# Performance work log

Measured on AMD Instinct MI355X. Metric: run time of the kernel, lower is better.

Reference implementation:

```python
import jax, jax.numpy as jnp
import numpy as np

IN_F, OUT_F, RANK = 4096, 4096, 1024
B, S_LEN = 4, 2048


def _dequant(data, scale, zp):
    # (int_data - zero_point) * scale, per-tensor scalar quantization
    return (data.astype(jnp.float32) - zp.astype(jnp.float32)) * scale.astype(jnp.float32)


def setup_inputs() -> dict:
    key = jax.random.key(0)
    ks = jax.random.split(key, 8)
    x = jax.random.normal(ks[0], (B, S_LEN, IN_F), dtype=jnp.float32)
    U_data = jax.random.randint(ks[1], (OUT_F, RANK), 0, 255, dtype=jnp.int32)
    S_data = jax.random.randint(ks[2], (RANK,), 0, 255, dtype=jnp.int32)
    Vh_data = jax.random.randint(ks[3], (RANK, IN_F), 0, 255, dtype=jnp.int32)
    bias = jax.random.normal(ks[4], (OUT_F,), dtype=jnp.float32)
    return {
        "x": x,
        "U_data": U_data,
        "U_scale": jnp.array([0.02], dtype=jnp.float32),
        "U_zp": jnp.array([128.0], dtype=jnp.float32),
        "S_data": S_data,
        "S_scale": jnp.array([0.05], dtype=jnp.float32),
        "S_zp": jnp.array([128.0], dtype=jnp.float32),
        "Vh_data": Vh_data,
        "Vh_scale": jnp.array([0.02], dtype=jnp.float32),
        "Vh_zp": jnp.array([128.0], dtype=jnp.float32),
        "bias": bias,
    }


def reference(x, U_data, U_scale, U_zp, S_data, S_scale, S_zp,
              Vh_data, Vh_scale, Vh_zp, bias):
    U = _dequant(U_data, U_scale, U_zp)     # [out, r]
    S = _dequant(S_data, S_scale, S_zp)     # [r]
    Vh = _dequant(Vh_data, Vh_scale, Vh_zp)  # [r, in]
    orig_shape = x.shape
    x_flat = x.reshape(-1, orig_shape[-1])  # [N, in]
    h = x_flat @ Vh.T                        # [N, r]
    h = h * S[None, :]
    y = h @ U.T                              # [N, out]
    y = y + bias
    return y.reshape(orig_shape[:-1] + (U.shape[0],))
```

## Files before the change

kernel.cpp:

```cpp
#include <hip/hip_runtime.h>
#include <stdint.h>

#define NROWS 8192
#define INF   4096
#define OUTF  4096
#define RNK   1024

typedef unsigned short u16;
typedef __attribute__((ext_vector_type(8))) short bf16x8;
typedef __attribute__((ext_vector_type(4))) float f32x4;
typedef __attribute__((ext_vector_type(8))) unsigned short u16x8;

__device__ __forceinline__ u16 f32_bf16(float f) {
  union { float f; uint32_t u; } v; v.f = f;
  return (u16)((v.u + 0x7FFF + ((v.u >> 16) & 1)) >> 16);
}


__global__ __launch_bounds__(256) void convert_x(const float* __restrict__ x,
                                                 u16* __restrict__ o) {
  int t = blockIdx.x * 256 + threadIdx.x;
  int e = t * 8;
  float4 a = *(const float4*)(x + e);
  float4 b = *(const float4*)(x + e + 4);
  u16x8 r;
  r[0] = f32_bf16(a.x); r[1] = f32_bf16(a.y); r[2] = f32_bf16(a.z); r[3] = f32_bf16(a.w);
  r[4] = f32_bf16(b.x); r[5] = f32_bf16(b.y); r[6] = f32_bf16(b.z); r[7] = f32_bf16(b.w);
  *(u16x8*)(o + e) = r;
}

__global__ __launch_bounds__(256) void dequant_vh(const int* __restrict__ vh,
                                                  const float* __restrict__ vs,
                                                  const float* __restrict__ vz,
                                                  const int* __restrict__ sd,
                                                  const float* __restrict__ ss,
                                                  const float* __restrict__ sz,
                                                  u16* __restrict__ o) {
  int t = blockIdx.x * 256 + threadIdx.x;
  int e = t * 4;
  int row = e >> 12;
  float sval = ((float)sd[row] - sz[0]) * ss[0];
  float sc = vs[0] * sval;
  float zp = vz[0];
  int4 d = *(const int4*)(vh + e);
  ushort4 r;
  r.x = f32_bf16(((float)d.x - zp) * sc);
  r.y = f32_bf16(((float)d.y - zp) * sc);
  r.z = f32_bf16(((float)d.z - zp) * sc);
  r.w = f32_bf16(((float)d.w - zp) * sc);
  *(ushort4*)(o + e) = r;
}

__global__ __launch_bounds__(256) void dequant_u(const int* __restrict__ ud,
                                                 const float* __restrict__ us,
                                                 const float* __restrict__ uz,
                                                 u16* __restrict__ o) {
  int t = blockIdx.x * 256 + threadIdx.x;
  int e = t * 4;
  float sc = us[0];
  float zp = uz[0];
  int4 d = *(const int4*)(ud + e);
  ushort4 r;
  r.x = f32_bf16(((float)d.x - zp) * sc);
  r.y = f32_bf16(((float)d.y - zp) * sc);
  r.z = f32_bf16(((float)d.z - zp) * sc);
  r.w = f32_bf16(((float)d.w - zp) * sc);
  *(ushort4*)(o + e) = r;
}


__device__ __forceinline__ void gl_lds16(const u16* g, u16* l) {
  __builtin_amdgcn_global_load_lds(
      (const __attribute__((address_space(1))) void*)g,
      (__attribute__((address_space(3))) void*)l, 16, 0, 0);
}

template <bool OUT_BF16, bool ADD_BIAS>
__global__ __launch_bounds__(256) void gemm_bt(const u16* __restrict__ A,
                                               const u16* __restrict__ B,
                                               void* __restrict__ Cv,
                                               const float* __restrict__ bias,
                                               const int N, const int K) {
  constexpr int BM = 128, BN = 128, BK = 64;
  __shared__ __attribute__((aligned(16))) u16 ldsA[BM * BK];
  __shared__ __attribute__((aligned(16))) u16 ldsB[BN * BK];

  const int tid  = threadIdx.x;
  const int lane = tid & 63;
  const int wave = tid >> 6;
  const int bm = blockIdx.y * BM;
  const int bn = blockIdx.x * BN;
  const int wm = (wave >> 1) * 64;
  const int wn = (wave & 1) * 64;

  f32x4 acc[4][4] = {};

  const int srow = tid >> 3;
  const int scol = (((tid & 7) ^ (srow & 7)) * 8);
  const int lcol = (tid & 7) * 8;
  const u16* gA = A + (bm + srow) * K + scol;
  const u16* gB = B + (bn + srow) * K + scol;
  u16* lA = ldsA + srow * BK + lcol;
  u16* lB = ldsB + srow * BK + lcol;

  for (int kt = 0; kt < K; kt += BK) {
#pragma unroll
    for (int i = 0; i < 4; ++i) {
      gl_lds16(gA + i * 32 * K + kt, lA + i * 32 * BK);
      gl_lds16(gB + i * 32 * K + kt, lB + i * 32 * BK);
    }
    __syncthreads();

    const int r  = lane & 15;
    const int kq = (lane >> 4) * 8;
#pragma unroll
    for (int ks = 0; ks < BK; ks += 32) {
      const int pcol = (((ks + kq) >> 3) ^ (r & 7)) << 3;
      bf16x8 af[4], bfr[4];
#pragma unroll
      for (int i = 0; i < 4; ++i)
        af[i] = *(const bf16x8*)(ldsA + (wm + i * 16 + r) * BK + pcol);
#pragma unroll
      for (int j = 0; j < 4; ++j)
        bfr[j] = *(const bf16x8*)(ldsB + (wn + j * 16 + r) * BK + pcol);
#pragma unroll
      for (int i = 0; i < 4; ++i)
#pragma unroll
        for (int j = 0; j < 4; ++j)
          acc[i][j] = __builtin_amdgcn_mfma_f32_16x16x32_bf16(af[i], bfr[j], acc[i][j], 0, 0, 0);
    }
    __syncthreads();
  }

  const int col0 = lane & 15;
  const int row0 = (lane >> 4) * 4;
#pragma unroll
  for (int i = 0; i < 4; ++i) {
#pragma unroll
    for (int j = 0; j < 4; ++j) {
      const int gcol = bn + wn + j * 16 + col0;
      float bv = 0.f;
      if (ADD_BIAS) bv = bias[gcol];
#pragma unroll
      for (int rr = 0; rr < 4; ++rr) {
        const int grow = bm + wm + i * 16 + row0 + rr;
        float v = acc[i][j][rr] + bv;
        if (OUT_BF16)
          ((u16*)Cv)[grow * N + gcol] = f32_bf16(v);
        else
          ((float*)Cv)[grow * N + gcol] = v;
      }
    }
  }
}


extern "C" void kernel_launch(void* const* d_in, const int* in_sizes, int n_in,
                              void* d_out, int out_size, void* d_ws, size_t ws_size,
                              hipStream_t stream) {
  const float* x        = (const float*)d_in[0];
  const int*   U_data   = (const int*)d_in[1];
  const float* U_scale  = (const float*)d_in[2];
  const float* U_zp     = (const float*)d_in[3];
  const int*   S_data   = (const int*)d_in[4];
  const float* S_scale  = (const float*)d_in[5];
  const float* S_zp     = (const float*)d_in[6];
  const int*   Vh_data  = (const int*)d_in[7];
  const float* Vh_scale = (const float*)d_in[8];
  const float* Vh_zp    = (const float*)d_in[9];
  const float* bias     = (const float*)d_in[10];
  float* out = (float*)d_out;

  char* ws = (char*)d_ws;
  u16* xb  = (u16*)ws;
  u16* vhb = (u16*)(ws + (size_t)67108864);
  u16* ub  = (u16*)(ws + (size_t)67108864 + 8388608);
  u16* hb  = (u16*)(ws + (size_t)67108864 + 16777216);

  convert_x<<<NROWS * INF / (8 * 256), 256, 0, stream>>>(x, xb);
  dequant_vh<<<RNK * INF / (4 * 256), 256, 0, stream>>>(Vh_data, Vh_scale, Vh_zp,
                                                        S_data, S_scale, S_zp, vhb);
  dequant_u<<<OUTF * RNK / (4 * 256), 256, 0, stream>>>(U_data, U_scale, U_zp, ub);

  gemm_bt<true, false><<<dim3(RNK / 128, NROWS / 128), 256, 0, stream>>>(
      xb, vhb, (void*)hb, nullptr, RNK, INF);
  gemm_bt<false, true><<<dim3(OUTF / 128, NROWS / 128), 256, 0, stream>>>(
      hb, ub, (void*)out, bias, OUTF, RNK);
}
```

Before: 425.6 us.

## Replace GEMM with 8-wave double-buffered pipelined kernel using larger tiles

Replaces the simple single-buffered 128x128 GEMM with a 512-thread, 256xBN tile kernel that double-buffers LDS and splits each K step into four phases. Each phase issues the async global-to-LDS loads for the next stage while running MFMAs on the current one, with explicit vmcnt waits, barriers and setprio. The aim is to hide global load latency and raise arithmetic intensity through larger tiles. In exchange it uses more LDS and registers and depends on correct hand-written wait counts.

```diff
diff --git a/kernel.cpp b/kernel.cpp
--- a/kernel.cpp
+++ b/kernel.cpp
@@ -75,83 +75,151 @@
       (__attribute__((address_space(3))) void*)l, 16, 0, 0);
 }
 
-template <bool OUT_BF16, bool ADD_BIAS>
-__global__ __launch_bounds__(256) void gemm_bt(const u16* __restrict__ A,
-                                               const u16* __restrict__ B,
-                                               void* __restrict__ Cv,
-                                               const float* __restrict__ bias,
-                                               const int N, const int K) {
-  constexpr int BM = 128, BN = 128, BK = 64;
-  __shared__ __attribute__((aligned(16))) u16 ldsA[BM * BK];
-  __shared__ __attribute__((aligned(16))) u16 ldsB[BN * BK];
+template <int VM> __device__ __forceinline__ void vm_wait() {
+  static_assert(VM == 3 || VM == 4, "unexpected vmcnt");
+  if constexpr (VM == 3) asm volatile("s_waitcnt vmcnt(3)" ::: "memory");
+  if constexpr (VM == 4) asm volatile("s_waitcnt vmcnt(4)" ::: "memory");
+}
+
+template <int BN, int K, int N, bool OUT_BF16, bool ADD_BIAS>
+__global__ __launch_bounds__(512, 2) void gemm8p(const u16* __restrict__ A,
+                                                 const u16* __restrict__ B,
+                                                 void* __restrict__ Cv,
+                                                 const float* __restrict__ bias) {
+  constexpr int BM = 256, BK = 64;
+  constexpr int WN = BN / 4;
+  constexpr int QJ = WN / 32;
+  constexpr int LB = (BN == 256) ? 2 : 1;
+  constexpr int NT = K / BK;
+  constexpr int AH = 128 * BK;
+  constexpr int BH = (BN / 2) * BK;
+
+  __shared__ __attribute__((aligned(16))) u16 ldsA[2 * 2 * AH];
+  __shared__ __attribute__((aligned(16))) u16 ldsB[2 * 2 * BH];
 
   const int tid  = threadIdx.x;
   const int lane = tid & 63;
   const int wave = tid >> 6;
-  const int bm = blockIdx.y * BM;
-  const int bn = blockIdx.x * BN;
-  const int wm = (wave >> 1) * 64;
-  const int wn = (wave & 1) * 64;
-
-  f32x4 acc[4][4] = {};
+  const int wm   = wave >> 2;
+  const int wn   = wave & 3;
+  const int bm   = blockIdx.y * BM;
+  const int bn   = blockIdx.x * BN;
 
   const int srow = tid >> 3;
-  const int scol = (((tid & 7) ^ (srow & 7)) * 8);
-  const int lcol = (tid & 7) * 8;
-  const u16* gA = A + (bm + srow) * K + scol;
-  const u16* gB = B + (bn + srow) * K + scol;
-  u16* lA = ldsA + srow * BK + lcol;
-  u16* lB = ldsB + srow * BK + lcol;
-
-  for (int kt = 0; kt < K; kt += BK) {
-#pragma unroll
-    for (int i = 0; i < 4; ++i) {
-      gl_lds16(gA + i * 32 * K + kt, lA + i * 32 * BK);
-      gl_lds16(gB + i * 32 * K + kt, lB + i * 32 * BK);
-    }
-    __syncthreads();
-
-    const int r  = lane & 15;
-    const int kq = (lane >> 4) * 8;
-#pragma unroll
-    for (int ks = 0; ks < BK; ks += 32) {
-      const int pcol = (((ks + kq) >> 3) ^ (r & 7)) << 3;
-      bf16x8 af[4], bfr[4];
-#pragma unroll
-      for (int i = 0; i < 4; ++i)
-        af[i] = *(const bf16x8*)(ldsA + (wm + i * 16 + r) * BK + pcol);
-#pragma unroll
-      for (int j = 0; j < 4; ++j)
-        bfr[j] = *(const bf16x8*)(ldsB + (wn + j * 16 + r) * BK + pcol);
-#pragma unroll
-      for (int i = 0; i < 4; ++i)
-#pragma unroll
-        for (int j = 0; j < 4; ++j)
-          acc[i][j] = __builtin_amdgcn_mfma_f32_16x16x32_bf16(af[i], bfr[j], acc[i][j], 0, 0, 0);
-    }
-    __syncthreads();
+  const int spc  = tid & 7;
+  const int sgc  = spc ^ (srow & 7);
+
+  const u16* gA = A + (size_t)(bm + srow) * K + sgc * 8;
+  const u16* gB = B + (size_t)(bn + srow) * K + sgc * 8;
+  u16* lA = ldsA + srow * BK + spc * 8;
+  u16* lB = ldsB + srow * BK + spc * 8;
+
+#define STAGE_A(buf, h, kt)                                                    \
+  { const u16* g_ = gA + (size_t)(h) * 128 * K + (kt);                         \
+    u16* l_ = lA + ((buf) * 2 + (h)) * AH;                                     \
+    gl_lds16(g_, l_);                                                          \
+    gl_lds16(g_ + (size_t)64 * K, l_ + 64 * BK); }
+
+#define STAGE_B(buf, h, kt)                                                    \
+  { const u16* g_ = gB + (size_t)(h) * (BN / 2) * K + (kt);                    \
+    u16* l_ = lB + ((buf) * 2 + (h)) * BH;                                     \
+    gl_lds16(g_, l_);                                                          \
+    if constexpr (LB == 2) gl_lds16(g_ + (size_t)64 * K, l_ + 64 * BK); }
+
+  const int r   = lane & 15;
+  const int kq  = (lane >> 4) * 8;
+  const int pc0 = (((kq) >> 3) ^ (r & 7)) << 3;
+  const int pc1 = (((32 + kq) >> 3) ^ (r & 7)) << 3;
+
+  f32x4 acc[2][2][4][QJ] = {};
+
+#define PHASE(buf, qm, qn, STAGE, VMW)                                         \
+  {                                                                            \
+    bf16x8 af[4][2], bfr[QJ][2];                                               \
+    const u16* abase = ldsA + ((buf) * 2 + (qm)) * AH + (wm * 64 + r) * BK;    \
+    _Pragma("unroll")                                                          \
+    for (int i = 0; i < 4; ++i) {                                              \
+      af[i][0] = *(const bf16x8*)(abase + i * 16 * BK + pc0);                  \
+      af[i][1] = *(const bf16x8*)(abase + i * 16 * BK + pc1);                  \
+    }                                                                          \
+    const u16* bbase =                                                         \
+        ldsB + ((buf) * 2 + (qn)) * BH + (wn * (WN / 2) + r) * BK;             \
+    _Pragma("unroll")                                                          \
+    for (int j = 0; j < QJ; ++j) {                                             \
+      bfr[j][0] = *(const bf16x8*)(bbase + j * 16 * BK + pc0);                 \
+      bfr[j][1] = *(const bf16x8*)(bbase + j * 16 * BK + pc1);                 \
+    }                                                                          \
+    STAGE;                                                                     \
+    __builtin_amdgcn_sched_barrier(0);                                         \
+    __builtin_amdgcn_s_barrier();                                              \
+    __builtin_amdgcn_sched_barrier(0);                                         \
+    __builtin_amdgcn_s_setprio(1);                                             \
+    _Pragma("unroll")                                                          \
+    for (int i = 0; i < 4; ++i)                                                \
+      _Pragma("unroll")                                                        \
+      for (int j = 0; j < QJ; ++j) {                                           \
+        acc[qm][qn][i][j] = __builtin_amdgcn_mfma_f32_16x16x32_bf16(           \
+            af[i][0], bfr[j][0], acc[qm][qn][i][j], 0, 0, 0);                  \
+        acc[qm][qn][i][j] = __builtin_amdgcn_mfma_f32_16x16x32_bf16(           \
+            af[i][1], bfr[j][1], acc[qm][qn][i][j], 0, 0, 0);                  \
+      }                                                                        \
+    __builtin_amdgcn_s_setprio(0);                                             \
+    __builtin_amdgcn_sched_barrier(0);                                         \
+    VMW;                                                                       \
+    __builtin_amdgcn_s_barrier();                                              \
+    __builtin_amdgcn_sched_barrier(0);                                         \
+  }
+
+  STAGE_A(0, 0, 0);
+  STAGE_B(0, 0, 0);
+  STAGE_B(0, 1, 0);
+  STAGE_A(0, 1, 0);
+  __builtin_amdgcn_sched_barrier(0);
+  constexpr int KT1 = (NT > 1 ? BK : 0);
+  STAGE_A(1, 0, KT1);
+  STAGE_B(1, 0, KT1);
+  __builtin_amdgcn_sched_barrier(0);
+  vm_wait<2 + LB>();
+  __builtin_amdgcn_s_barrier();
+  __builtin_amdgcn_sched_barrier(0);
+
+  for (int t = 0; t < NT; ++t) {
+    const int buf  = t & 1;
+    const int nbuf = buf ^ 1;
+    const int kt1 = (t + 1 < NT ? t + 1 : NT - 1) * BK;
+    const int kt2 = (t + 2 < NT ? t + 2 : NT - 1) * BK;
+    PHASE(buf, 0, 0, STAGE_B(nbuf, 1, kt1), );
+    PHASE(buf, 0, 1, STAGE_A(nbuf, 1, kt1), );
+    PHASE(buf, 1, 0, STAGE_A(buf, 0, kt2), );
+    PHASE(buf, 1, 1, STAGE_B(buf, 0, kt2), (vm_wait<2 + LB>()));
   }
 
   const int col0 = lane & 15;
   const int row0 = (lane >> 4) * 4;
 #pragma unroll
-  for (int i = 0; i < 4; ++i) {
-#pragma unroll
-    for (int j = 0; j < 4; ++j) {
-      const int gcol = bn + wn + j * 16 + col0;
-      float bv = 0.f;
-      if (ADD_BIAS) bv = bias[gcol];
-#pragma unroll
-      for (int rr = 0; rr < 4; ++rr) {
-        const int grow = bm + wm + i * 16 + row0 + rr;
-        float v = acc[i][j][rr] + bv;
-        if (OUT_BF16)
-          ((u16*)Cv)[grow * N + gcol] = f32_bf16(v);
-        else
-          ((float*)Cv)[grow * N + gcol] = v;
+  for (int qm = 0; qm < 2; ++qm)
+#pragma unroll
+    for (int qn = 0; qn < 2; ++qn)
+#pragma unroll
+      for (int j = 0; j < QJ; ++j) {
+        const int gcol = bn + (qn * 4 + wn) * (WN / 2) + j * 16 + col0;
+        float bv = 0.f;
+        if constexpr (ADD_BIAS) bv = bias[gcol];
+#pragma unroll
+        for (int i = 0; i < 4; ++i)
+#pragma unroll
+          for (int rr = 0; rr < 4; ++rr) {
+            const int grow = bm + qm * 128 + wm * 64 + i * 16 + row0 + rr;
+            float v = acc[qm][qn][i][j][rr] + bv;
+            if constexpr (OUT_BF16)
+              ((u16*)Cv)[(size_t)grow * N + gcol] = f32_bf16(v);
+            else
+              ((float*)Cv)[(size_t)grow * N + gcol] = v;
+          }
       }
-    }
-  }
+#undef PHASE
+#undef STAGE_A
+#undef STAGE_B
 }
 
 
@@ -182,8 +250,9 @@
                                                         S_data, S_scale, S_zp, vhb);
   dequant_u<<<OUTF * RNK / (4 * 256), 256, 0, stream>>>(U_data, U_scale, U_zp, ub);
 
-  gemm_bt<true, false><<<dim3(RNK / 128, NROWS / 128), 256, 0, stream>>>(
-      xb, vhb, (void*)hb, nullptr, RNK, INF);
-  gemm_bt<false, true><<<dim3(OUTF / 128, NROWS / 128), 256, 0, stream>>>(
-      hb, ub, (void*)out, bias, OUTF, RNK);
-}
+  gemm8p<128, INF, RNK, true, false>
+      <<<dim3(RNK / 128, NROWS / 256), 512, 0, stream>>>(xb, vhb, (void*)hb, nullptr);
+
+  gemm8p<256, RNK, OUTF, false, true>
+      <<<dim3(OUTF / 256, NROWS / 256), 512, 0, stream>>>(hb, ub, (void*)out, bias);
+}
```

New measurement: 491.5 us. +15.5%, slower.
